# Performance work log

Measured on AMD Instinct MI355X. Metric: run time of the kernel, lower is better.

Reference implementation:

```python
import jax, jax.numpy as jnp
import numpy as np

NUM_HEADS = 12
TOP_R = 0.1


def attention_rollout(attn_stack):
    # attn_stack: [L, B, H, N1, N1]; head_fusion='mean'
    A = attn_stack.mean(axis=2)                       # [L, B, N1, N1]
    n1 = A.shape[-1]
    A = A + jnp.eye(n1, dtype=A.dtype)                # residual connection
    A = A / A.sum(axis=-1, keepdims=True)             # row-normalize
    rollout = A[0]
    for l in range(1, A.shape[0]):                    # small fixed loop over layers
        rollout = A[l] @ rollout
    return rollout                                    # [B, N1, N1]


def setup_inputs() -> dict:
    key = jax.random.key(0)
    ks = jax.random.split(key, 7)
    B, N1, D, L, H = 32, 197, 768, 12, NUM_HEADS
    s = 1.0 / np.sqrt(D)
    return {
        "x": jax.random.normal(ks[0], (B, N1, D), dtype=jnp.float32),
        "attn_stack": jax.random.uniform(ks[1], (L, B, H, N1, N1), dtype=jnp.float32),
        "q_w": jax.random.normal(ks[2], (D, D), dtype=jnp.float32) * s,
        "k_w": jax.random.normal(ks[3], (D, D), dtype=jnp.float32) * s,
        "v_w": jax.random.normal(ks[4], (D, D), dtype=jnp.float32) * s,
        "proj_w": jax.random.normal(ks[5], (D, D), dtype=jnp.float32) * s,
        "proj_b": jnp.zeros((D,), dtype=jnp.float32),
    }


def reference(x, attn_stack, q_w, k_w, v_w, proj_w, proj_b):
    B, N1, C = x.shape
    N = N1 - 1
    H = NUM_HEADS
    hd = C // H
    scale = hd ** (-0.5)

    # --- attention rollout (detached in original) -> CLS attention over patches ---
    rollout = attention_rollout(jax.lax.stop_gradient(attn_stack))  # [B, N1, N1]
    cls_attention = rollout[:, 0, 1:]                               # [B, N]
    R = int(N * TOP_R)                                              # static top-R count
    _, top_indices = jax.lax.top_k(cls_attention, R)                # [B, R]

    # --- gather top-R local tokens (shift by 1 to skip CLS) ---
    x_local = jnp.take_along_axis(x, (top_indices + 1)[:, :, None], axis=1)  # [B, R, C]

    # --- projections ---
    q = (x_local @ q_w.T).reshape(B, R, H, hd).transpose(0, 2, 1, 3)   # [B, H, R, hd]
    k = (x @ k_w.T).reshape(B, N1, H, hd).transpose(0, 2, 1, 3)        # [B, H, N1, hd]
    v = (x @ v_w.T).reshape(B, N1, H, hd).transpose(0, 2, 1, 3)        # [B, H, N1, hd]

    # --- cross attention: local queries vs global key/values ---
    attn = jnp.einsum('bhrd,bhnd->bhrn', q, k) * scale                 # [B, H, R, N1]
    attn = jax.nn.softmax(attn, axis=-1)
    out = jnp.einsum('bhrn,bhnd->bhrd', attn, v)                       # [B, H, R, hd]
    out = out.transpose(0, 2, 1, 3).reshape(B, R, C)

    # --- output projection ---
    out = out @ proj_w.T + proj_b
    return out
```

## Files before the change

kernel.cpp:

```cpp
#include <hip/hip_runtime.h>
#include <math.h>

#define L_  12
#define B_  32
#define H_  12
#define N1_ 197
#define D_  768
#define R_  19
#define M_TOK (B_ * N1_)
#define NN (N1_ * N1_)

#define K1_FULL_ROWS  69344
#define K1_ROWS       69376
#define K1_BLOCKS     (K1_ROWS / 4)
#define PACK_ROWS     (M_TOK + 2304)
#define PACK_BLOCKS   ((PACK_ROWS * 24 + 255) / 256)

typedef __attribute__((ext_vector_type(8))) short short8;
typedef __attribute__((ext_vector_type(4))) float f32x4;

__device__ __forceinline__ f32x4 ld4u(const float* p) {
  f32x4 r; __builtin_memcpy(&r, p, 16); return r;
}
__device__ __forceinline__ void st4u(float* p, f32x4 v) {
  __builtin_memcpy(p, &v, 16);
}

__device__ inline ushort f2bf_rn(float f) {
  unsigned u = __float_as_uint(f);
  unsigned r = (u + 0x7FFFu + ((u >> 16) & 1u)) >> 16;
  return (ushort)r;
}
__device__ inline float bf2f(ushort h) { return __uint_as_float((unsigned)h << 16); }
__device__ inline void cvt4(float4 f, ushort4& h, ushort4& l) {
  h.x = f2bf_rn(f.x); l.x = f2bf_rn(f.x - bf2f(h.x));
  h.y = f2bf_rn(f.y); l.y = f2bf_rn(f.y - bf2f(h.y));
  h.z = f2bf_rn(f.z); l.z = f2bf_rn(f.z - bf2f(h.z));
  h.w = f2bf_rn(f.w); l.w = f2bf_rn(f.w - bf2f(h.w));
}

typedef const __attribute__((address_space(1))) void* as1_vp;
typedef __attribute__((address_space(3))) void* as3_vp;
__device__ __forceinline__ void gl_lds16(const void* g, void* s) {
  __builtin_amdgcn_global_load_lds((as1_vp)g, (as3_vp)s, 16, 0, 0);
}

__global__ __launch_bounds__(256) void mega_k1_pack(const float* __restrict__ attn,
                                                    float* __restrict__ P,
                                                    float* __restrict__ dvec,
                                                    const float* __restrict__ x,
                                                    const float* __restrict__ k_w,
                                                    const float* __restrict__ v_w,
                                                    const float* __restrict__ q_w,
                                                    ushort* __restrict__ xpack,
                                                    ushort* __restrict__ wpack) {
  int bid = blockIdx.x;
  if (bid < K1_BLOCKS) {
    int wid = threadIdx.x >> 6;
    int t   = threadIdx.x & 63;
    int row_id = bid * 4 + wid;
    int l, b, i;
    if (row_id < K1_FULL_ROWS) {
      l = row_id / 6304;
      int rem = row_id - l * 6304;
      b = rem / 197;
      i = rem - b * 197;
    } else {
      l = 11; b = row_id - K1_FULL_ROWS; i = 0;
    }
    int lb   = l * B_ + b;
    int prow = lb * N1_ + i;
    const float* base = attn + (size_t)lb * (H_ * NN) + (size_t)i * N1_;
    f32x4 acc = {0.f, 0.f, 0.f, 0.f};
    if (t < 49) {
      const float* p = base + 4 * t;
#pragma unroll
      for (int h = 0; h < H_; ++h) acc += ld4u(p + (size_t)h * NN);
    } else if (t == 49) {
      const float* p = base + 196;
#pragma unroll
      for (int h = 0; h < H_; ++h) acc.x += p[(size_t)h * NN];
    }
    float s = (acc.x + acc.y) + (acc.z + acc.w);
#pragma unroll
    for (int o = 32; o; o >>= 1) s += __shfl_xor(s, o);
    float inv = 1.f / (s + 12.f);
    float* Pr = P + (size_t)prow * N1_;
    if (t < 49)       st4u(Pr + 4 * t, acc * inv);
    else if (t == 49) Pr[196] = acc.x * inv;
    if (t == 0) dvec[prow] = 12.f * inv;
  } else {
    int t = (bid - K1_BLOCKS) * 256 + threadIdx.x;
    if (t >= PACK_ROWS * 24) return;
    int row = t / 24, kb = t - row * 24;
    const float* src;
    ushort* dst;
    if (row < M_TOK) {
      src = x + (size_t)row * D_;
      dst = xpack + (size_t)row * 1536;
    } else {
      int wr = row - M_TOK;
      int g = wr / 768, rl = wr - g * 768;
      const float* wsrc = (g == 0) ? k_w : (g == 1) ? v_w : q_w;
      src = wsrc + (size_t)rl * D_;
      dst = wpack + (size_t)wr * 1536;
    }
    src += kb * 32;
    dst += kb * 64;
#pragma unroll
    for (int u = 0; u < 8; ++u) {
      float4 f = *(const float4*)(src + u * 4);
      ushort4 h, l2; cvt4(f, h, l2);
      *(ushort4*)(dst + u * 4)      = h;
      *(ushort4*)(dst + 32 + u * 4) = l2;
    }
  }
}

__global__ __launch_bounds__(1024) void k2_chain_topk(const float* __restrict__ P,
                                                      const float* __restrict__ dvec,
                                                      int* __restrict__ gidx) {
  int b = blockIdx.x;
  __shared__ float v[N1_];
  __shared__ float part[4][N1_];
  int t = threadIdx.x, quar = t >> 8, j = t & 255;

  if (t < N1_) {
    const float* Pr = P + ((size_t)(11 * B_ + b) * N1_) * N1_;
    v[t] = Pr[t] + (t == 0 ? dvec[(11 * B_ + b) * N1_] : 0.f);
  }
  __syncthreads();

  for (int l = 10; l >= 0; --l) {
    if (j < N1_) {
      const float* Pc = P + ((size_t)(l * B_ + b) * N1_) * N1_ + j;
      float a[8] = {0.f, 0.f, 0.f, 0.f, 0.f, 0.f, 0.f, 0.f};
      int ibeg = (quar * N1_) / 4;
      int iend = ((quar + 1) * N1_) / 4;
      int i = ibeg;
      for (; i + 8 <= iend; i += 8) {
#pragma unroll
        for (int u = 0; u < 8; ++u)
          a[u] += v[i + u] * Pc[(size_t)(i + u) * N1_];
      }
      for (; i < iend; ++i) a[0] += v[i] * Pc[(size_t)i * N1_];
      float s = ((a[0] + a[1]) + (a[2] + a[3])) + ((a[4] + a[5]) + (a[6] + a[7]));
      if (quar == 0) s += v[j] * dvec[(l * B_ + b) * N1_ + j];
      part[quar][j] = s;
    }
    __syncthreads();
    if (t < N1_) v[t] = (part[0][t] + part[1][t]) + (part[2][t] + part[3][t]);
    __syncthreads();
  }

  if (t < 64) {
    float val[4];
    int   idx[4];
#pragma unroll
    for (int c = 0; c < 4; ++c) {
      int n = t + c * 64;
      bool ok = (n < N1_ - 1);
      val[c] = ok ? v[n + 1] : -1e30f;
      idx[c] = ok ? n : (1 << 20);
    }
    for (int r = 0; r < R_; ++r) {
      float bv = val[0];
      int   bi = idx[0];
#pragma unroll
      for (int c = 1; c < 4; ++c)
        if (val[c] > bv || (val[c] == bv && idx[c] < bi)) { bv = val[c]; bi = idx[c]; }
#pragma unroll
      for (int o = 32; o; o >>= 1) {
        float ov = __shfl_xor(bv, o);
        int   oi = __shfl_xor(bi, o);
        if (ov > bv || (ov == bv && oi < bi)) { bv = ov; bi = oi; }
      }
      if (t == 0) gidx[b * R_ + r] = b * N1_ + bi + 1;
#pragma unroll
      for (int c = 0; c < 4; ++c)
        if (idx[c] == bi) val[c] = -1e30f;
    }
  }
}

__global__ __launch_bounds__(256) void gemm_kvq_fast(const ushort* __restrict__ xpack,
                                                     const ushort* __restrict__ wpack,
                                                     const int* __restrict__ gidx,
                                                     float* __restrict__ kvb,
                                                     float* __restrict__ qbuf) {
  __shared__ __attribute__((aligned(16))) ushort As[128 * 64];
  __shared__ __attribute__((aligned(16))) ushort Bs[128 * 64];
  int tid = threadIdx.x, lane = tid & 63, wid = tid >> 6;
  int wr = wid >> 1, wc = wid & 1;
  int lr = lane & 15, lk = lane >> 4;

  int bid = blockIdx.x;
  int bm, wrow0, ccol0, ldc, Mrows;
  float* C;
  bool gath;
  if (bid < 600) {
    bm = bid % 50; int bn = bid / 50;
    wrow0 = bn * 128; ccol0 = bn * 128; ldc = 1536; Mrows = M_TOK;
    C = kvb; gath = false;
  } else {
    int tq = bid - 600;
    bm = tq % 5; int bn = tq / 5;
    wrow0 = 1536 + bn * 128; ccol0 = bn * 128; ldc = 768; Mrows = 608;
    C = qbuf; gath = true;
  }

  const ushort* asrc[4];
  const ushort* bsrc[4];
  ushort* adst[4];
  ushort* bdst[4];
  int lrow = lane >> 3, cpr = lane & 7;
#pragma unroll
  for (int i = 0; i < 4; ++i) {
    int r_loc = wid * 32 + i * 8 + lrow;
    int c     = cpr ^ (r_loc & 7);
    int ga    = bm * 128 + r_loc; if (ga >= Mrows) ga = Mrows - 1;
    int arow  = gath ? gidx[ga] : ga;
    asrc[i] = xpack + (size_t)arow * 1536 + c * 8;
    bsrc[i] = wpack + (size_t)(wrow0 + r_loc) * 1536 + c * 8;
    adst[i] = &As[(wid * 32 + i * 8) * 64];
    bdst[i] = &Bs[(wid * 32 + i * 8) * 64];
  }

  int oh = (lk ^ (lr & 7)) * 8;
  int ol = oh ^ 32;

  f32x4 acc[4][4] = {};

#pragma unroll
  for (int i = 0; i < 4; ++i) { gl_lds16(asrc[i], adst[i]); gl_lds16(bsrc[i], bdst[i]); }

  for (int kb = 0; kb < 24; ++kb) {
    __syncthreads();
    short8 afh[4], afl[4], bfh[4], bfl[4];
#pragma unroll
    for (int m = 0; m < 4; ++m) {
      const ushort* rp = &As[(wr * 64 + m * 16 + lr) * 64];
      afh[m] = *(const short8*)(rp + oh);
      afl[m] = *(const short8*)(rp + ol);
    }
#pragma unroll
    for (int n = 0; n < 4; ++n) {
      const ushort* rp = &Bs[(wc * 64 + n * 16 + lr) * 64];
      bfh[n] = *(const short8*)(rp + oh);
      bfl[n] = *(const short8*)(rp + ol);
    }
    __syncthreads();
    if (kb < 23) {
#pragma unroll
      for (int i = 0; i < 4; ++i) {
        gl_lds16(asrc[i] + (kb + 1) * 64, adst[i]);
        gl_lds16(bsrc[i] + (kb + 1) * 64, bdst[i]);
      }
    }
#pragma unroll
    for (int m = 0; m < 4; ++m)
#pragma unroll
      for (int n = 0; n < 4; ++n) {
        acc[m][n] = __builtin_amdgcn_mfma_f32_16x16x32_bf16(afh[m], bfh[n], acc[m][n], 0, 0, 0);
        acc[m][n] = __builtin_amdgcn_mfma_f32_16x16x32_bf16(afh[m], bfl[n], acc[m][n], 0, 0, 0);
        acc[m][n] = __builtin_amdgcn_mfma_f32_16x16x32_bf16(afl[m], bfh[n], acc[m][n], 0, 0, 0);
      }
  }

#pragma unroll
  for (int m = 0; m < 4; ++m) {
    int row0 = bm * 128 + wr * 64 + m * 16 + (lane >> 4) * 4;
#pragma unroll
    for (int i = 0; i < 4; ++i) {
      int row = row0 + i;
      if (row < Mrows) {
#pragma unroll
        for (int n = 0; n < 4; ++n) {
          int col = ccol0 + wc * 64 + n * 16 + lr;
          C[(size_t)row * ldc + col] = acc[m][n][i];
        }
      }
    }
  }
}

#define PK 40
template <int BM, int BN, int MF, int NF>
__global__ __launch_bounds__(256) void gemm_f32in(const float* __restrict__ A,
                                                  const float* __restrict__ W0,
                                                  const float* __restrict__ bias,
                                                  float* __restrict__ C,
                                                  int M, int K, int ldc) {
  __shared__ __attribute__((aligned(16))) ushort As[2][BM][PK];
  __shared__ __attribute__((aligned(16))) ushort Bs[2][BN][PK];
  constexpr int TPRA = 256 / BM;
  constexpr int EPTA = 32 / TPRA;
  constexpr int NA4  = EPTA / 4;
  constexpr int TPRB = 256 / BN;
  constexpr int EPTB = 32 / TPRB;
  constexpr int NB4  = EPTB / 4;

  int tid  = threadIdx.x;
  int lane = tid & 63, wid = tid >> 6;
  int wr = wid >> 1, wc = wid & 1;
  int lr = lane & 15, lk = lane >> 4;
  int bm = blockIdx.x, bn = blockIdx.y;

  int arow_s = tid / TPRA;
  int akoff  = (tid % TPRA) * EPTA;
  int ar = bm * BM + arow_s; if (ar >= M) ar = M - 1;
  const float* ap = A + (size_t)ar * K + akoff;

  int brow_s = tid / TPRB;
  int bkoff  = (tid % TPRB) * EPTB;
  int wrow   = bn * BN + brow_s;
  const float* wp = W0 + (size_t)wrow * K + bkoff;

  f32x4 acc[MF][NF] = {};

  float4 pa[NA4], pb[NB4];
#pragma unroll
  for (int u = 0; u < NA4; ++u) pa[u] = *(const float4*)(ap + u * 4);
#pragma unroll
  for (int u = 0; u < NB4; ++u) pb[u] = *(const float4*)(wp + u * 4);

  for (int k0 = 0; k0 < K; k0 += 32) {
#pragma unroll
    for (int u = 0; u < NA4; ++u) {
      ushort4 h, l; cvt4(pa[u], h, l);
      *(ushort4*)&As[0][arow_s][akoff + u * 4] = h;
      *(ushort4*)&As[1][arow_s][akoff + u * 4] = l;
    }
#pragma unroll
    for (int u = 0; u < NB4; ++u) {
      ushort4 h, l; cvt4(pb[u], h, l);
      *(ushort4*)&Bs[0][brow_s][bkoff + u * 4] = h;
      *(ushort4*)&Bs[1][brow_s][bkoff + u * 4] = l;
    }
    __syncthreads();

    int kn = k0 + 32;
    if (kn < K) {
#pragma unroll
      for (int u = 0; u < NA4; ++u) pa[u] = *(const float4*)(ap + kn + u * 4);
#pragma unroll
      for (int u = 0; u < NB4; ++u) pb[u] = *(const float4*)(wp + kn + u * 4);
    }

    short8 af[2][MF], bf[2][NF];
#pragma unroll
    for (int m = 0; m < MF; ++m) {
      af[0][m] = *(const short8*)&As[0][wr * (BM / 2) + m * 16 + lr][lk * 8];
      af[1][m] = *(const short8*)&As[1][wr * (BM / 2) + m * 16 + lr][lk * 8];
    }
#pragma unroll
    for (int n = 0; n < NF; ++n) {
      bf[0][n] = *(const short8*)&Bs[0][wc * (BN / 2) + n * 16 + lr][lk * 8];
      bf[1][n] = *(const short8*)&Bs[1][wc * (BN / 2) + n * 16 + lr][lk * 8];
    }
#pragma unroll
    for (int m = 0; m < MF; ++m)
#pragma unroll
      for (int n = 0; n < NF; ++n) {
        acc[m][n] = __builtin_amdgcn_mfma_f32_16x16x32_bf16(af[0][m], bf[0][n], acc[m][n], 0, 0, 0);
        acc[m][n] = __builtin_amdgcn_mfma_f32_16x16x32_bf16(af[0][m], bf[1][n], acc[m][n], 0, 0, 0);
        acc[m][n] = __builtin_amdgcn_mfma_f32_16x16x32_bf16(af[1][m], bf[0][n], acc[m][n], 0, 0, 0);
      }
    __syncthreads();
  }

#pragma unroll
  for (int m = 0; m < MF; ++m) {
    int row0 = bm * BM + wr * (BM / 2) + m * 16 + lk * 4;
#pragma unroll
    for (int i = 0; i < 4; ++i) {
      int row = row0 + i;
      if (row < M) {
#pragma unroll
        for (int n = 0; n < NF; ++n) {
          int col = bn * BN + wc * (BN / 2) + n * 16 + lr;
          float vv = acc[m][n][i];
          if (bias) vv += bias[col];
          C[(size_t)row * ldc + col] = vv;
        }
      }
    }
  }
}

__global__ __launch_bounds__(256) void k5_attn(const float* __restrict__ kvb,
                                               const float* __restrict__ qb,
                                               float* __restrict__ ctx) {
  int bh = blockIdx.x;
  int b = bh / H_, h = bh % H_;
  __shared__ float ks[N1_][68];
  __shared__ float qs[R_][64];
  __shared__ float sc[R_][200];
  __shared__ float rsum[R_];
  int t = threadIdx.x;
  int lane = t & 63, wid = t >> 6;

  const float* kbase = kvb + (size_t)b * N1_ * 1536 + h * 64;
  for (int n = wid; n < N1_; n += 4)
    ks[n][lane] = kbase[(size_t)n * 1536 + lane];
  const float* qrow = qb + (size_t)b * R_ * D_ + h * 64;
  for (int e = t; e < R_ * 64; e += 256) {
    int r = e >> 6, d = e & 63;
    qs[r][d] = qrow[(size_t)r * D_ + d];
  }
  __syncthreads();

  if (t < N1_) {
    float accr[R_];
#pragma unroll
    for (int r = 0; r < R_; ++r) accr[r] = 0.f;
#pragma unroll
    for (int d0 = 0; d0 < 4; ++d0) {
      float4 k0 = *(const float4*)&ks[t][d0 * 16 + 0];
      float4 k1 = *(const float4*)&ks[t][d0 * 16 + 4];
      float4 k2 = *(const float4*)&ks[t][d0 * 16 + 8];
      float4 k3 = *(const float4*)&ks[t][d0 * 16 + 12];
#pragma unroll
      for (int r = 0; r < R_; ++r) {
        float4 q0 = *(const float4*)&qs[r][d0 * 16 + 0];
        float4 q1 = *(const float4*)&qs[r][d0 * 16 + 4];
        float4 q2 = *(const float4*)&qs[r][d0 * 16 + 8];
        float4 q3 = *(const float4*)&qs[r][d0 * 16 + 12];
        accr[r] += k0.x * q0.x + k0.y * q0.y + k0.z * q0.z + k0.w * q0.w
                 + k1.x * q1.x + k1.y * q1.y + k1.z * q1.z + k1.w * q1.w
                 + k2.x * q2.x + k2.y * q2.y + k2.z * q2.z + k2.w * q2.w
                 + k3.x * q3.x + k3.y * q3.y + k3.z * q3.z + k3.w * q3.w;
      }
    }
#pragma unroll
    for (int r = 0; r < R_; ++r) sc[r][t] = accr[r] * 0.125f;
  }
  __syncthreads();

  for (int r = wid; r < R_; r += 4) {
    float x0 = sc[r][lane];
    float x1 = sc[r][lane + 64];
    float x2 = sc[r][lane + 128];
    bool ok3 = (lane + 192 < N1_);
    float x3 = ok3 ? sc[r][lane + 192] : -1e30f;
    float m = fmaxf(fmaxf(x0, x1), fmaxf(x2, x3));
#pragma unroll
    for (int o = 32; o; o >>= 1) m = fmaxf(m, __shfl_xor(m, o));
    float e0 = expf(x0 - m), e1 = expf(x1 - m), e2 = expf(x2 - m);
    float e3 = ok3 ? expf(x3 - m) : 0.f;
    float s = e0 + e1 + e2 + e3;
#pragma unroll
    for (int o = 32; o; o >>= 1) s += __shfl_xor(s, o);
    sc[r][lane] = e0; sc[r][lane + 64] = e1; sc[r][lane + 128] = e2;
    if (ok3) sc[r][lane + 192] = e3;
    if (lane == 0) rsum[r] = s;
  }
  __syncthreads();

  const float* vb = kvb + (size_t)b * N1_ * 1536 + 768 + h * 64 + lane;
  int r0 = wid, r1 = wid + 4, r2 = wid + 8, r3 = wid + 12, r4 = wid + 16;
  bool has4 = (r4 < R_);
  float a0 = 0.f, a1 = 0.f, a2 = 0.f, a3 = 0.f, a4 = 0.f;
#pragma unroll 4
  for (int n = 0; n < N1_; ++n) {
    float vv = vb[(size_t)n * 1536];
    a0 += sc[r0][n] * vv;
    a1 += sc[r1][n] * vv;
    a2 += sc[r2][n] * vv;
    a3 += sc[r3][n] * vv;
    if (has4) a4 += sc[r4][n] * vv;
  }
  float* cb = ctx + (size_t)(b * R_) * D_ + h * 64 + lane;
  cb[(size_t)r0 * D_] = a0 / rsum[r0];
  cb[(size_t)r1 * D_] = a1 / rsum[r1];
  cb[(size_t)r2 * D_] = a2 / rsum[r2];
  cb[(size_t)r3 * D_] = a3 / rsum[r3];
  if (has4) cb[(size_t)r4 * D_] = a4 / rsum[r4];
}

extern "C" void kernel_launch(void* const* d_in, const int* in_sizes, int n_in,
                              void* d_out, int out_size, void* d_ws, size_t ws_size,
                              hipStream_t stream) {
  const float* x      = (const float*)d_in[0];
  const float* attn   = (const float*)d_in[1];
  const float* q_w    = (const float*)d_in[2];
  const float* k_w    = (const float*)d_in[3];
  const float* v_w    = (const float*)d_in[4];
  const float* proj_w = (const float*)d_in[5];
  const float* proj_b = (const float*)d_in[6];
  float* out = (float*)d_out;

  char* w = (char*)d_ws;
  auto take = [&](size_t bytes) { char* p = w; w += (bytes + 255) & ~(size_t)255; return p; };
  float*  P     = (float*)take((size_t)L_ * B_ * N1_ * N1_ * 4);
  float*  dvec  = (float*)take((size_t)L_ * B_ * N1_ * 4);
  int*    gidx  = (int*)take(B_ * R_ * 4);
  float*  kvb   = (float*)take((size_t)M_TOK * 1536 * 4);
  float*  qbuf  = (float*)take((size_t)B_ * R_ * D_ * 4);
  float*  ctx   = (float*)take((size_t)B_ * R_ * D_ * 4);
  ushort* xpack = (ushort*)take((size_t)M_TOK * 1536 * 2);
  ushort* wpack = (ushort*)take((size_t)2304 * 1536 * 2);

  hipLaunchKernelGGL(mega_k1_pack, dim3(K1_BLOCKS + PACK_BLOCKS), dim3(256), 0,
                     stream, attn, P, dvec, x, k_w, v_w, q_w, xpack, wpack);
  hipLaunchKernelGGL(k2_chain_topk, dim3(B_), dim3(1024), 0, stream, P, dvec, gidx);
  hipLaunchKernelGGL(gemm_kvq_fast, dim3(630), dim3(256), 0, stream,
                     xpack, wpack, gidx, kvb, qbuf);
  hipLaunchKernelGGL(k5_attn, dim3(B_ * H_), dim3(256), 0, stream, kvb, qbuf, ctx);
  hipLaunchKernelGGL((gemm_f32in<64, 64, 2, 2>), dim3(10, 12), dim3(256), 0, stream,
                     ctx, proj_w, proj_b, out, B_ * R_, D_, D_);
}
```

Baseline: 346.2 us.

## Overlap rollout chain with full QKV GEMM and regroup head-mean rows per block

The rollout chain and top-k now run in the same launch as the QKV projection GEMM, so the serial 32-block chain overlaps the GEMM tiles instead of gating them. To make this possible, Q is computed for every token (a 2304-wide GEMM), and the attention kernel gathers the selected Q rows itself. This removes the gather dependency but adds about a third more GEMM work for Q rows that are never used. The head-mean kernel now processes four contiguous rows per 256-thread block through shared memory, and the chain uses one thread per column with a fully unrolled loop instead of splitting rows four ways.

```diff
diff --git a/kernel.cpp b/kernel.cpp
--- a/kernel.cpp
+++ b/kernel.cpp
@@ -10,11 +10,14 @@
 #define M_TOK (B_ * N1_)
 #define NN (N1_ * N1_)
 
-#define K1_FULL_ROWS  69344
-#define K1_ROWS       69376
-#define K1_BLOCKS     (K1_ROWS / 4)
+#define K1_LB_BLOCKS  (11 * 32 * 50)
+#define K1V2_BLOCKS   (K1_LB_BLOCKS + 32)
 #define PACK_ROWS     (M_TOK + 2304)
 #define PACK_BLOCKS   ((PACK_ROWS * 24 + 255) / 256)
+#define MEGA1_BLOCKS  (K1V2_BLOCKS + PACK_BLOCKS)
+
+#define QKV_TILES     900
+#define MEGA2_BLOCKS  (QKV_TILES + B_)
 
 typedef __attribute__((ext_vector_type(8))) short short8;
 typedef __attribute__((ext_vector_type(4))) float f32x4;
@@ -45,52 +48,79 @@
   __builtin_amdgcn_global_load_lds((as1_vp)g, (as3_vp)s, 16, 0, 0);
 }
 
-__global__ __launch_bounds__(256) void mega_k1_pack(const float* __restrict__ attn,
-                                                    float* __restrict__ P,
-                                                    float* __restrict__ dvec,
-                                                    const float* __restrict__ x,
-                                                    const float* __restrict__ k_w,
-                                                    const float* __restrict__ v_w,
-                                                    const float* __restrict__ q_w,
-                                                    ushort* __restrict__ xpack,
-                                                    ushort* __restrict__ wpack) {
+__global__ __launch_bounds__(256) void mega1_k1_pack(const float* __restrict__ attn,
+                                                     float* __restrict__ P,
+                                                     float* __restrict__ dvec,
+                                                     const float* __restrict__ x,
+                                                     const float* __restrict__ k_w,
+                                                     const float* __restrict__ v_w,
+                                                     const float* __restrict__ q_w,
+                                                     ushort* __restrict__ xpack,
+                                                     ushort* __restrict__ wpack) {
   int bid = blockIdx.x;
-  if (bid < K1_BLOCKS) {
-    int wid = threadIdx.x >> 6;
-    int t   = threadIdx.x & 63;
-    int row_id = bid * 4 + wid;
-    int l, b, i;
-    if (row_id < K1_FULL_ROWS) {
-      l = row_id / 6304;
-      int rem = row_id - l * 6304;
-      b = rem / 197;
-      i = rem - b * 197;
+  if (bid < K1V2_BLOCKS) {
+    __shared__ float lrow[800];
+    int l, b, i0, nrows;
+    if (bid < K1_LB_BLOCKS) {
+      int lb  = bid / 50;
+      int sub = bid - lb * 50;
+      l = lb >> 5; b = lb & 31;
+      i0 = sub * 4;
+      nrows = (i0 + 4 <= N1_) ? 4 : (N1_ - i0);
     } else {
-      l = 11; b = row_id - K1_FULL_ROWS; i = 0;
-    }
-    int lb   = l * B_ + b;
-    int prow = lb * N1_ + i;
-    const float* base = attn + (size_t)lb * (H_ * NN) + (size_t)i * N1_;
+      l = 11; b = bid - K1_LB_BLOCKS; i0 = 0; nrows = 1;
+    }
+    int lbi = l * B_ + b;
+    const float* base = attn + (size_t)lbi * (H_ * NN) + (size_t)i0 * N1_;
+    int W = nrows * N1_;
+    int t = threadIdx.x;
     f32x4 acc = {0.f, 0.f, 0.f, 0.f};
-    if (t < 49) {
+    if (4 * t + 4 <= W) {
       const float* p = base + 4 * t;
 #pragma unroll
       for (int h = 0; h < H_; ++h) acc += ld4u(p + (size_t)h * NN);
-    } else if (t == 49) {
-      const float* p = base + 196;
-#pragma unroll
-      for (int h = 0; h < H_; ++h) acc.x += p[(size_t)h * NN];
-    }
-    float s = (acc.x + acc.y) + (acc.z + acc.w);
-#pragma unroll
-    for (int o = 32; o; o >>= 1) s += __shfl_xor(s, o);
-    float inv = 1.f / (s + 12.f);
-    float* Pr = P + (size_t)prow * N1_;
-    if (t < 49)       st4u(Pr + 4 * t, acc * inv);
-    else if (t == 49) Pr[196] = acc.x * inv;
-    if (t == 0) dvec[prow] = 12.f * inv;
+    } else if (4 * t < W) {
+      const float* p = base + 4 * t;
+      int rem = W - 4 * t;
+#pragma unroll
+      for (int h = 0; h < H_; ++h) {
+        const float* ph = p + (size_t)h * NN;
+        for (int e = 0; e < rem; ++e) acc[e] += ph[e];
+      }
+    }
+    if (4 * t < W) {
+      lrow[4 * t]     = acc.x;
+      lrow[4 * t + 1] = acc.y;
+      lrow[4 * t + 2] = acc.z;
+      lrow[4 * t + 3] = acc.w;
+    }
+    __syncthreads();
+    int wv = t >> 6, ln = t & 63;
+    if (wv < nrows) {
+      int rb = N1_ * wv;
+      float s0 = 0.f, s1 = 0.f, s2 = 0.f, s3 = 0.f;
+      if (ln < 49) {
+        s0 = lrow[rb + 4 * ln];     s1 = lrow[rb + 4 * ln + 1];
+        s2 = lrow[rb + 4 * ln + 2]; s3 = lrow[rb + 4 * ln + 3];
+      } else if (ln == 49) {
+        s0 = lrow[rb + 196];
+      }
+      float s = (s0 + s1) + (s2 + s3);
+#pragma unroll
+      for (int o = 32; o; o >>= 1) s += __shfl_xor(s, o);
+      float inv = 1.f / (s + 12.f);
+      int prow = lbi * N1_ + i0 + wv;
+      float* Pr = P + (size_t)prow * N1_;
+      if (ln < 49) {
+        f32x4 vv = {s0 * inv, s1 * inv, s2 * inv, s3 * inv};
+        st4u(Pr + 4 * ln, vv);
+      } else if (ln == 49) {
+        Pr[196] = s0 * inv;
+      }
+      if (ln == 0) dvec[prow] = 12.f * inv;
+    }
   } else {
-    int t = (bid - K1_BLOCKS) * 256 + threadIdx.x;
+    int t = (bid - K1V2_BLOCKS) * 256 + threadIdx.x;
     if (t >= PACK_ROWS * 24) return;
     int row = t / 24, kb = t - row * 24;
     const float* src;
@@ -117,171 +147,246 @@
   }
 }
 
-__global__ __launch_bounds__(1024) void k2_chain_topk(const float* __restrict__ P,
-                                                      const float* __restrict__ dvec,
-                                                      int* __restrict__ gidx) {
-  int b = blockIdx.x;
-  __shared__ float v[N1_];
-  __shared__ float part[4][N1_];
-  int t = threadIdx.x, quar = t >> 8, j = t & 255;
+__global__ __launch_bounds__(256) void mega2_qkv_chain(const ushort* __restrict__ xpack,
+                                                       const ushort* __restrict__ wpack,
+                                                       const float* __restrict__ P,
+                                                       const float* __restrict__ dvec,
+                                                       float* __restrict__ qkv,
+                                                       int* __restrict__ gidx) {
+  int bid = blockIdx.x;
+  if (bid < QKV_TILES) {
+    __shared__ __attribute__((aligned(16))) ushort As[128 * 64];
+    __shared__ __attribute__((aligned(16))) ushort Bs[128 * 64];
+    int tid = threadIdx.x, lane = tid & 63, wid = tid >> 6;
+    int wr = wid >> 1, wc = wid & 1;
+    int lr = lane & 15, lk = lane >> 4;
+    int bm = bid % 50, bn = bid / 50;
+
+    const ushort* asrc[4];
+    const ushort* bsrc[4];
+    ushort* adst[4];
+    ushort* bdst[4];
+    int lrow = lane >> 3, cpr = lane & 7;
+#pragma unroll
+    for (int i = 0; i < 4; ++i) {
+      int r_loc = wid * 32 + i * 8 + lrow;
+      int c     = cpr ^ (r_loc & 7);
+      int ga    = bm * 128 + r_loc; if (ga >= M_TOK) ga = M_TOK - 1;
+      asrc[i] = xpack + (size_t)ga * 1536 + c * 8;
+      bsrc[i] = wpack + (size_t)(bn * 128 + r_loc) * 1536 + c * 8;
+      adst[i] = &As[(wid * 32 + i * 8) * 64];
+      bdst[i] = &Bs[(wid * 32 + i * 8) * 64];
+    }
+    int oh = (lk ^ (lr & 7)) * 8;
+    int ol = oh ^ 32;
+
+    f32x4 acc[4][4] = {};
+#pragma unroll
+    for (int i = 0; i < 4; ++i) { gl_lds16(asrc[i], adst[i]); gl_lds16(bsrc[i], bdst[i]); }
+
+    for (int kb = 0; kb < 24; ++kb) {
+      __syncthreads();
+      short8 afh[4], afl[4], bfh[4], bfl[4];
+#pragma unroll
+      for (int m = 0; m < 4; ++m) {
+        const ushort* rp = &As[(wr * 64 + m * 16 + lr) * 64];
+        afh[m] = *(const short8*)(rp + oh);
+        afl[m] = *(const short8*)(rp + ol);
+      }
+#pragma unroll
+      for (int n = 0; n < 4; ++n) {
+        const ushort* rp = &Bs[(wc * 64 + n * 16 + lr) * 64];
+        bfh[n] = *(const short8*)(rp + oh);
+        bfl[n] = *(const short8*)(rp + ol);
+      }
+      __syncthreads();
+      if (kb < 23) {
+#pragma unroll
+        for (int i = 0; i < 4; ++i) {
+          gl_lds16(asrc[i] + (kb + 1) * 64, adst[i]);
+          gl_lds16(bsrc[i] + (kb + 1) * 64, bdst[i]);
+        }
+      }
+#pragma unroll
+      for (int m = 0; m < 4; ++m)
+#pragma unroll
+        for (int n = 0; n < 4; ++n) {
+          acc[m][n] = __builtin_amdgcn_mfma_f32_16x16x32_bf16(afh[m], bfh[n], acc[m][n], 0, 0, 0);
+          acc[m][n] = __builtin_amdgcn_mfma_f32_16x16x32_bf16(afh[m], bfl[n], acc[m][n], 0, 0, 0);
+          acc[m][n] = __builtin_amdgcn_mfma_f32_16x16x32_bf16(afl[m], bfh[n], acc[m][n], 0, 0, 0);
+        }
+    }
+
+#pragma unroll
+    for (int m = 0; m < 4; ++m) {
+      int row0 = bm * 128 + wr * 64 + m * 16 + (lane >> 4) * 4;
+#pragma unroll
+      for (int i = 0; i < 4; ++i) {
+        int row = row0 + i;
+        if (row < M_TOK) {
+#pragma unroll
+          for (int n = 0; n < 4; ++n) {
+            int col = bn * 128 + wc * 64 + n * 16 + lr;
+            qkv[(size_t)row * 2304 + col] = acc[m][n][i];
+          }
+        }
+      }
+    }
+  } else {
+    int b = bid - QKV_TILES;
+    __shared__ float v[200];
+    int t = threadIdx.x;
+    if (t < 200) {
+      if (t < N1_) {
+        const float* Pr = P + ((size_t)(11 * B_ + b) * N1_) * N1_;
+        v[t] = Pr[t] + (t == 0 ? dvec[(11 * B_ + b) * N1_] : 0.f);
+      } else {
+        v[t] = 0.f;
+      }
+    }
+    __syncthreads();
+
+    for (int l = 10; l >= 0; --l) {
+      float res = 0.f;
+      if (t < N1_) {
+        const float* Pc = P + ((size_t)(l * B_ + b) * N1_) * N1_ + t;
+        float a[8] = {0.f, 0.f, 0.f, 0.f, 0.f, 0.f, 0.f, 0.f};
+#pragma unroll
+        for (int g = 0; g < 24; ++g) {
+#pragma unroll
+          for (int u = 0; u < 8; ++u)
+            a[u] += v[g * 8 + u] * Pc[(size_t)(g * 8 + u) * N1_];
+        }
+#pragma unroll
+        for (int u = 0; u < 5; ++u)
+          a[u] += v[192 + u] * Pc[(size_t)(192 + u) * N1_];
+        res = ((a[0] + a[1]) + (a[2] + a[3])) + ((a[4] + a[5]) + (a[6] + a[7]));
+        res += v[t] * dvec[(l * B_ + b) * N1_ + t];
+      }
+      __syncthreads();
+      if (t < N1_) v[t] = res;
+      __syncthreads();
+    }
+
+    if (t < 64) {
+      float val[4];
+      int   idx[4];
+#pragma unroll
+      for (int c = 0; c < 4; ++c) {
+        int n = t + c * 64;
+        bool ok = (n < N1_ - 1);
+        val[c] = ok ? v[n + 1] : -1e30f;
+        idx[c] = ok ? n : (1 << 20);
+      }
+      for (int r = 0; r < R_; ++r) {
+        float bv = val[0];
+        int   bi = idx[0];
+#pragma unroll
+        for (int c = 1; c < 4; ++c)
+          if (val[c] > bv || (val[c] == bv && idx[c] < bi)) { bv = val[c]; bi = idx[c]; }
+#pragma unroll
+        for (int o = 32; o; o >>= 1) {
+          float ov = __shfl_xor(bv, o);
+          int   oi = __shfl_xor(bi, o);
+          if (ov > bv || (ov == bv && oi < bi)) { bv = ov; bi = oi; }
+        }
+        if (t == 0) gidx[b * R_ + r] = b * N1_ + bi + 1;
+#pragma unroll
+        for (int c = 0; c < 4; ++c)
+          if (idx[c] == bi) val[c] = -1e30f;
+      }
+    }
+  }
+}
+
+__global__ __launch_bounds__(256) void k5_attn(const float* __restrict__ qkv,
+                                               const int* __restrict__ gidx,
+                                               float* __restrict__ ctx) {
+  int bh = blockIdx.x;
+  int b = bh / H_, h = bh % H_;
+  __shared__ float ks[N1_][68];
+  __shared__ float qs[R_][64];
+  __shared__ float sc[R_][200];
+  __shared__ float rsum[R_];
+  int t = threadIdx.x;
+  int lane = t & 63, wid = t >> 6;
+
+  const float* kbase = qkv + (size_t)(b * N1_) * 2304 + h * 64;
+  for (int n = wid; n < N1_; n += 4)
+    ks[n][lane] = kbase[(size_t)n * 2304 + lane];
+  for (int e = t; e < R_ * 64; e += 256) {
+    int r = e >> 6, d = e & 63;
+    int grow = gidx[b * R_ + r];
+    qs[r][d] = qkv[(size_t)grow * 2304 + 1536 + h * 64 + d];
+  }
+  __syncthreads();
 
   if (t < N1_) {
-    const float* Pr = P + ((size_t)(11 * B_ + b) * N1_) * N1_;
-    v[t] = Pr[t] + (t == 0 ? dvec[(11 * B_ + b) * N1_] : 0.f);
+    float accr[R_];
+#pragma unroll
+    for (int r = 0; r < R_; ++r) accr[r] = 0.f;
+#pragma unroll
+    for (int d0 = 0; d0 < 4; ++d0) {
+      float4 k0 = *(const float4*)&ks[t][d0 * 16 + 0];
+      float4 k1 = *(const float4*)&ks[t][d0 * 16 + 4];
+      float4 k2 = *(const float4*)&ks[t][d0 * 16 + 8];
+      float4 k3 = *(const float4*)&ks[t][d0 * 16 + 12];
+#pragma unroll
+      for (int r = 0; r < R_; ++r) {
+        float4 q0 = *(const float4*)&qs[r][d0 * 16 + 0];
+        float4 q1 = *(const float4*)&qs[r][d0 * 16 + 4];
+        float4 q2 = *(const float4*)&qs[r][d0 * 16 + 8];
+        float4 q3 = *(const float4*)&qs[r][d0 * 16 + 12];
+        accr[r] += k0.x * q0.x + k0.y * q0.y + k0.z * q0.z + k0.w * q0.w
+                 + k1.x * q1.x + k1.y * q1.y + k1.z * q1.z + k1.w * q1.w
+                 + k2.x * q2.x + k2.y * q2.y + k2.z * q2.z + k2.w * q2.w
+                 + k3.x * q3.x + k3.y * q3.y + k3.z * q3.z + k3.w * q3.w;
+      }
+    }
+#pragma unroll
+    for (int r = 0; r < R_; ++r) sc[r][t] = accr[r] * 0.125f;
   }
   __syncthreads();
 
-  for (int l = 10; l >= 0; --l) {
-    if (j < N1_) {
-      const float* Pc = P + ((size_t)(l * B_ + b) * N1_) * N1_ + j;
-      float a[8] = {0.f, 0.f, 0.f, 0.f, 0.f, 0.f, 0.f, 0.f};
-      int ibeg = (quar * N1_) / 4;
-      int iend = ((quar + 1) * N1_) / 4;
-      int i = ibeg;
-      for (; i + 8 <= iend; i += 8) {
-#pragma unroll
-        for (int u = 0; u < 8; ++u)
-          a[u] += v[i + u] * Pc[(size_t)(i + u) * N1_];
-      }
-      for (; i < iend; ++i) a[0] += v[i] * Pc[(size_t)i * N1_];
-      float s = ((a[0] + a[1]) + (a[2] + a[3])) + ((a[4] + a[5]) + (a[6] + a[7]));
-      if (quar == 0) s += v[j] * dvec[(l * B_ + b) * N1_ + j];
-      part[quar][j] = s;
-    }
-    __syncthreads();
-    if (t < N1_) v[t] = (part[0][t] + part[1][t]) + (part[2][t] + part[3][t]);
-    __syncthreads();
-  }
-
-  if (t < 64) {
-    float val[4];
-    int   idx[4];
-#pragma unroll
-    for (int c = 0; c < 4; ++c) {
-      int n = t + c * 64;
-      bool ok = (n < N1_ - 1);
-      val[c] = ok ? v[n + 1] : -1e30f;
-      idx[c] = ok ? n : (1 << 20);
-    }
-    for (int r = 0; r < R_; ++r) {
-      float bv = val[0];
-      int   bi = idx[0];
-#pragma unroll
-      for (int c = 1; c < 4; ++c)
-        if (val[c] > bv || (val[c] == bv && idx[c] < bi)) { bv = val[c]; bi = idx[c]; }
-#pragma unroll
-      for (int o = 32; o; o >>= 1) {
-        float ov = __shfl_xor(bv, o);
-        int   oi = __shfl_xor(bi, o);
-        if (ov > bv || (ov == bv && oi < bi)) { bv = ov; bi = oi; }
-      }
-      if (t == 0) gidx[b * R_ + r] = b * N1_ + bi + 1;
-#pragma unroll
-      for (int c = 0; c < 4; ++c)
-        if (idx[c] == bi) val[c] = -1e30f;
-    }
-  }
-}
-
-__global__ __launch_bounds__(256) void gemm_kvq_fast(const ushort* __restrict__ xpack,
-                                                     const ushort* __restrict__ wpack,
-                                                     const int* __restrict__ gidx,
-                                                     float* __restrict__ kvb,
-                                                     float* __restrict__ qbuf) {
-  __shared__ __attribute__((aligned(16))) ushort As[128 * 64];
-  __shared__ __attribute__((aligned(16))) ushort Bs[128 * 64];
-  int tid = threadIdx.x, lane = tid & 63, wid = tid >> 6;
-  int wr = wid >> 1, wc = wid & 1;
-  int lr = lane & 15, lk = lane >> 4;
-
-  int bid = blockIdx.x;
-  int bm, wrow0, ccol0, ldc, Mrows;
-  float* C;
-  bool gath;
-  if (bid < 600) {
-    bm = bid % 50; int bn = bid / 50;
-    wrow0 = bn * 128; ccol0 = bn * 128; ldc = 1536; Mrows = M_TOK;
-    C = kvb; gath = false;
-  } else {
-    int tq = bid - 600;
-    bm = tq % 5; int bn = tq / 5;
-    wrow0 = 1536 + bn * 128; ccol0 = bn * 128; ldc = 768; Mrows = 608;
-    C = qbuf; gath = true;
-  }
-
-  const ushort* asrc[4];
-  const ushort* bsrc[4];
-  ushort* adst[4];
-  ushort* bdst[4];
-  int lrow = lane >> 3, cpr = lane & 7;
-#pragma unroll
-  for (int i = 0; i < 4; ++i) {
-    int r_loc = wid * 32 + i * 8 + lrow;
-    int c     = cpr ^ (r_loc & 7);
-    int ga    = bm * 128 + r_loc; if (ga >= Mrows) ga = Mrows - 1;
-    int arow  = gath ? gidx[ga] : ga;
-    asrc[i] = xpack + (size_t)arow * 1536 + c * 8;
-    bsrc[i] = wpack + (size_t)(wrow0 + r_loc) * 1536 + c * 8;
-    adst[i] = &As[(wid * 32 + i * 8) * 64];
-    bdst[i] = &Bs[(wid * 32 + i * 8) * 64];
-  }
-
-  int oh = (lk ^ (lr & 7)) * 8;
-  int ol = oh ^ 32;
-
-  f32x4 acc[4][4] = {};
-
-#pragma unroll
-  for (int i = 0; i < 4; ++i) { gl_lds16(asrc[i], adst[i]); gl_lds16(bsrc[i], bdst[i]); }
-
-  for (int kb = 0; kb < 24; ++kb) {
-    __syncthreads();
-    short8 afh[4], afl[4], bfh[4], bfl[4];
-#pragma unroll
-    for (int m = 0; m < 4; ++m) {
-      const ushort* rp = &As[(wr * 64 + m * 16 + lr) * 64];
-      afh[m] = *(const short8*)(rp + oh);
-      afl[m] = *(const short8*)(rp + ol);
-    }
-#pragma unroll
-    for (int n = 0; n < 4; ++n) {
-      const ushort* rp = &Bs[(wc * 64 + n * 16 + lr) * 64];
-      bfh[n] = *(const short8*)(rp + oh);
-      bfl[n] = *(const short8*)(rp + ol);
-    }
-    __syncthreads();
-    if (kb < 23) {
-#pragma unroll
-      for (int i = 0; i < 4; ++i) {
-        gl_lds16(asrc[i] + (kb + 1) * 64, adst[i]);
-        gl_lds16(bsrc[i] + (kb + 1) * 64, bdst[i]);
-      }
-    }
-#pragma unroll
-    for (int m = 0; m < 4; ++m)
-#pragma unroll
-      for (int n = 0; n < 4; ++n) {
-        acc[m][n] = __builtin_amdgcn_mfma_f32_16x16x32_bf16(afh[m], bfh[n], acc[m][n], 0, 0, 0);
-        acc[m][n] = __builtin_amdgcn_mfma_f32_16x16x32_bf16(afh[m], bfl[n], acc[m][n], 0, 0, 0);
-        acc[m][n] = __builtin_amdgcn_mfma_f32_16x16x32_bf16(afl[m], bfh[n], acc[m][n], 0, 0, 0);
-      }
-  }
-
-#pragma unroll
-  for (int m = 0; m < 4; ++m) {
-    int row0 = bm * 128 + wr * 64 + m * 16 + (lane >> 4) * 4;
-#pragma unroll
-    for (int i = 0; i < 4; ++i) {
-      int row = row0 + i;
-      if (row < Mrows) {
-#pragma unroll
-        for (int n = 0; n < 4; ++n) {
-          int col = ccol0 + wc * 64 + n * 16 + lr;
-          C[(size_t)row * ldc + col] = acc[m][n][i];
-        }
-      }
-    }
-  }
+  for (int r = wid; r < R_; r += 4) {
+    float x0 = sc[r][lane];
+    float x1 = sc[r][lane + 64];
+    float x2 = sc[r][lane + 128];
+    bool ok3 = (lane + 192 < N1_);
+    float x3 = ok3 ? sc[r][lane + 192] : -1e30f;
+    float m = fmaxf(fmaxf(x0, x1), fmaxf(x2, x3));
+#pragma unroll
+    for (int o = 32; o; o >>= 1) m = fmaxf(m, __shfl_xor(m, o));
+    float e0 = expf(x0 - m), e1 = expf(x1 - m), e2 = expf(x2 - m);
+    float e3 = ok3 ? expf(x3 - m) : 0.f;
+    float s = e0 + e1 + e2 + e3;
+#pragma unroll
+    for (int o = 32; o; o >>= 1) s += __shfl_xor(s, o);
+    sc[r][lane] = e0; sc[r][lane + 64] = e1; sc[r][lane + 128] = e2;
+    if (ok3) sc[r][lane + 192] = e3;
+    if (lane == 0) rsum[r] = s;
+  }
+  __syncthreads();
+
+  const float* vb = qkv + (size_t)(b * N1_) * 2304 + 768 + h * 64 + lane;
+  int r0 = wid, r1 = wid + 4, r2 = wid + 8, r3 = wid + 12, r4 = wid + 16;
+  bool has4 = (r4 < R_);
+  float a0 = 0.f, a1 = 0.f, a2 = 0.f, a3 = 0.f, a4 = 0.f;
+#pragma unroll 4
+  for (int n = 0; n < N1_; ++n) {
+    float vv = vb[(size_t)n * 2304];
+    a0 += sc[r0][n] * vv;
+    a1 += sc[r1][n] * vv;
+    a2 += sc[r2][n] * vv;
+    a3 += sc[r3][n] * vv;
+    if (has4) a4 += sc[r4][n] * vv;
+  }
+  float* cb = ctx + (size_t)(b * R_) * D_ + h * 64 + lane;
+  cb[(size_t)r0 * D_] = a0 / rsum[r0];
+  cb[(size_t)r1 * D_] = a1 / rsum[r1];
+  cb[(size_t)r2 * D_] = a2 / rsum[r2];
+  cb[(size_t)r3 * D_] = a3 / rsum[r3];
+  if (has4) cb[(size_t)r4 * D_] = a4 / rsum[r4];
 }
 
 #define PK 40
@@ -388,96 +493,6 @@
   }
 }
 
-__global__ __launch_bounds__(256) void k5_attn(const float* __restrict__ kvb,
-                                               const float* __restrict__ qb,
-                                               float* __restrict__ ctx) {
-  int bh = blockIdx.x;
-  int b = bh / H_, h = bh % H_;
-  __shared__ float ks[N1_][68];
-  __shared__ float qs[R_][64];
-  __shared__ float sc[R_][200];
-  __shared__ float rsum[R_];
-  int t = threadIdx.x;
-  int lane = t & 63, wid = t >> 6;
-
-  const float* kbase = kvb + (size_t)b * N1_ * 1536 + h * 64;
-  for (int n = wid; n < N1_; n += 4)
-    ks[n][lane] = kbase[(size_t)n * 1536 + lane];
-  const float* qrow = qb + (size_t)b * R_ * D_ + h * 64;
-  for (int e = t; e < R_ * 64; e += 256) {
-    int r = e >> 6, d = e & 63;
-    qs[r][d] = qrow[(size_t)r * D_ + d];
-  }
-  __syncthreads();
-
-  if (t < N1_) {
-    float accr[R_];
-#pragma unroll
-    for (int r = 0; r < R_; ++r) accr[r] = 0.f;
-#pragma unroll
-    for (int d0 = 0; d0 < 4; ++d0) {
-      float4 k0 = *(const float4*)&ks[t][d0 * 16 + 0];
-      float4 k1 = *(const float4*)&ks[t][d0 * 16 + 4];
-      float4 k2 = *(const float4*)&ks[t][d0 * 16 + 8];
-      float4 k3 = *(const float4*)&ks[t][d0 * 16 + 12];
-#pragma unroll
-      for (int r = 0; r < R_; ++r) {
-        float4 q0 = *(const float4*)&qs[r][d0 * 16 + 0];
-        float4 q1 = *(const float4*)&qs[r][d0 * 16 + 4];
-        float4 q2 = *(const float4*)&qs[r][d0 * 16 + 8];
-        float4 q3 = *(const float4*)&qs[r][d0 * 16 + 12];
-        accr[r] += k0.x * q0.x + k0.y * q0.y + k0.z * q0.z + k0.w * q0.w
-                 + k1.x * q1.x + k1.y * q1.y + k1.z * q1.z + k1.w * q1.w
-                 + k2.x * q2.x + k2.y * q2.y + k2.z * q2.z + k2.w * q2.w
-                 + k3.x * q3.x + k3.y * q3.y + k3.z * q3.z + k3.w * q3.w;
-      }
-    }
-#pragma unroll
-    for (int r = 0; r < R_; ++r) sc[r][t] = accr[r] * 0.125f;
-  }
-  __syncthreads();
-
-  for (int r = wid; r < R_; r += 4) {
-    float x0 = sc[r][lane];
-    float x1 = sc[r][lane + 64];
-    float x2 = sc[r][lane + 128];
-    bool ok3 = (lane + 192 < N1_);
-    float x3 = ok3 ? sc[r][lane + 192] : -1e30f;
-    float m = fmaxf(fmaxf(x0, x1), fmaxf(x2, x3));
-#pragma unroll
-    for (int o = 32; o; o >>= 1) m = fmaxf(m, __shfl_xor(m, o));
-    float e0 = expf(x0 - m), e1 = expf(x1 - m), e2 = expf(x2 - m);
-    float e3 = ok3 ? expf(x3 - m) : 0.f;
-    float s = e0 + e1 + e2 + e3;
-#pragma unroll
-    for (int o = 32; o; o >>= 1) s += __shfl_xor(s, o);
-    sc[r][lane] = e0; sc[r][lane + 64] = e1; sc[r][lane + 128] = e2;
-    if (ok3) sc[r][lane + 192] = e3;
-    if (lane == 0) rsum[r] = s;
-  }
-  __syncthreads();
-
-  const float* vb = kvb + (size_t)b * N1_ * 1536 + 768 + h * 64 + lane;
-  int r0 = wid, r1 = wid + 4, r2 = wid + 8, r3 = wid + 12, r4 = wid + 16;
-  bool has4 = (r4 < R_);
-  float a0 = 0.f, a1 = 0.f, a2 = 0.f, a3 = 0.f, a4 = 0.f;
-#pragma unroll 4
-  for (int n = 0; n < N1_; ++n) {
-    float vv = vb[(size_t)n * 1536];
-    a0 += sc[r0][n] * vv;
-    a1 += sc[r1][n] * vv;
-    a2 += sc[r2][n] * vv;
-    a3 += sc[r3][n] * vv;
-    if (has4) a4 += sc[r4][n] * vv;
-  }
-  float* cb = ctx + (size_t)(b * R_) * D_ + h * 64 + lane;
-  cb[(size_t)r0 * D_] = a0 / rsum[r0];
-  cb[(size_t)r1 * D_] = a1 / rsum[r1];
-  cb[(size_t)r2 * D_] = a2 / rsum[r2];
-  cb[(size_t)r3 * D_] = a3 / rsum[r3];
-  if (has4) cb[(size_t)r4 * D_] = a4 / rsum[r4];
-}
-
 extern "C" void kernel_launch(void* const* d_in, const int* in_sizes, int n_in,
                               void* d_out, int out_size, void* d_ws, size_t ws_size,
                               hipStream_t stream) {
@@ -495,18 +510,16 @@
   float*  P     = (float*)take((size_t)L_ * B_ * N1_ * N1_ * 4);
   float*  dvec  = (float*)take((size_t)L_ * B_ * N1_ * 4);
   int*    gidx  = (int*)take(B_ * R_ * 4);
-  float*  kvb   = (float*)take((size_t)M_TOK * 1536 * 4);
-  float*  qbuf  = (float*)take((size_t)B_ * R_ * D_ * 4);
+  float*  qkv   = (float*)take((size_t)M_TOK * 2304 * 4);
   float*  ctx   = (float*)take((size_t)B_ * R_ * D_ * 4);
   ushort* xpack = (ushort*)take((size_t)M_TOK * 1536 * 2);
   ushort* wpack = (ushort*)take((size_t)2304 * 1536 * 2);
 
-  hipLaunchKernelGGL(mega_k1_pack, dim3(K1_BLOCKS + PACK_BLOCKS), dim3(256), 0,
-                     stream, attn, P, dvec, x, k_w, v_w, q_w, xpack, wpack);
-  hipLaunchKernelGGL(k2_chain_topk, dim3(B_), dim3(1024), 0, stream, P, dvec, gidx);
-  hipLaunchKernelGGL(gemm_kvq_fast, dim3(630), dim3(256), 0, stream,
-                     xpack, wpack, gidx, kvb, qbuf);
-  hipLaunchKernelGGL(k5_attn, dim3(B_ * H_), dim3(256), 0, stream, kvb, qbuf, ctx);
+  hipLaunchKernelGGL(mega1_k1_pack, dim3(MEGA1_BLOCKS), dim3(256), 0, stream,
+                     attn, P, dvec, x, k_w, v_w, q_w, xpack, wpack);
+  hipLaunchKernelGGL(mega2_qkv_chain, dim3(MEGA2_BLOCKS), dim3(256), 0, stream,
+                     xpack, wpack, P, dvec, qkv, gidx);
+  hipLaunchKernelGGL(k5_attn, dim3(B_ * H_), dim3(256), 0, stream, qkv, gidx, ctx);
   hipLaunchKernelGGL((gemm_f32in<64, 64, 2, 2>), dim3(10, 12), dim3(256), 0, stream,
                      ctx, proj_w, proj_b, out, B_ * R_, D_, D_);
 }
```

Result: slower. 387.0 us (+11.8%).
